# Performance work log

Hardware: AMD Instinct MI355X
Metric: run time of the kernel (lower is better)

The kernel has to match this reference:

```python
import jax, jax.numpy as jnp
import numpy as np

N_SIZE = 8
HIDDEN = 64
CELL = 1.0


def _social_pool(h, coords, mask):
    # h: [N, hid], coords: [N, 2], mask: [N] int
    N = coords.shape[0]
    rel = coords[None, :, :] - coords[:, None, :]            # rel[i, j] = coords[j] - coords[i]
    g = jnp.trunc(rel / CELL).astype(jnp.int32)              # python int() truncates toward zero
    half = N_SIZE // 2
    inb = (jnp.abs(g[..., 0]) <= half - 1) & (jnp.abs(g[..., 1]) <= half - 1)
    eye = jnp.eye(N, dtype=bool)
    m = mask != 0
    valid = inb & (~eye) & m[:, None] & m[None, :]           # [N, N]
    cell_idx = (g[..., 0] + half) * N_SIZE + (g[..., 1] + half)
    seg = jnp.arange(N, dtype=jnp.int32)[:, None] * (N_SIZE * N_SIZE) + jnp.where(valid, cell_idx, 0)
    contrib = jnp.where(valid[..., None], h[None, :, :], jnp.zeros((), h.dtype))  # [N, N, hid]
    H = jax.ops.segment_sum(contrib.reshape(N * N, -1), seg.reshape(-1),
                            num_segments=N * N_SIZE * N_SIZE)
    return H.reshape(N, N_SIZE * N_SIZE * h.shape[-1])


def _forward(X, part_masks, all_h_t, all_c_t, Y, T_pred,
             W_emb, b_emb, W_soc, b_soc, W_ih, b_ih, W_hh, b_hh, W_out, b_out):
    T, N = X.shape[0], X.shape[1]
    masks = part_masks[:, 0, :]                              # [T, N]
    masks_tm3 = jnp.concatenate([jnp.ones((3, N), masks.dtype), masks[:-3]], axis=0)
    ts = jnp.arange(T, dtype=jnp.int32)

    def step(carry, xs):
        h, c = carry
        x_t, mask_t, mask_tm3, y_t, t = xs
        coords = x_t[:, 2:]                                  # [N, 2]
        r = jax.nn.relu(coords @ W_emb + b_emb)              # Phi (dropout inactive in eval)
        H = _social_pool(h, coords, mask_t)
        e = jax.nn.relu(H @ W_soc + b_soc)
        z = jnp.concatenate([r, e], axis=1)
        gates = z @ W_ih + b_ih + h @ W_hh + b_hh            # torch LSTMCell gate order i,f,g,o
        i_g, f_g, g_g, o_g = jnp.split(gates, 4, axis=1)
        c_new = jax.nn.sigmoid(f_g) * c + jax.nn.sigmoid(i_g) * jnp.tanh(g_g)
        h_new = jax.nn.sigmoid(o_g) * jnp.tanh(c_new)
        out = (h_new @ W_out + b_out) * mask_t.astype(h.dtype)[:, None]
        appear = (t > 3) & (mask_t != 0) & (mask_tm3 == 0)
        out = jnp.where(appear[:, None], y_t, out)
        active = t <= T_pred                                 # frames beyond T_pred are skipped
        h2 = jnp.where(active, h_new, h)
        c2 = jnp.where(active, c_new, c)
        out = jnp.where(active, out, jnp.zeros_like(out))
        return (h2, c2), out

    (_, _), outputs = jax.lax.scan(step, (all_h_t, all_c_t), (X, masks, masks_tm3, Y, ts))
    return outputs


def setup_inputs() -> dict:
    key = jax.random.key(0)
    ks = jax.random.split(key, 16)
    T, N = 32, 1024
    inp = {
        "X": jax.random.normal(ks[0], (T, N, 4), jnp.float32),
        "part_masks": jax.random.randint(ks[1], (T, 1, N), 0, 2, jnp.int32),
        "all_h_t": jax.random.normal(ks[2], (N, HIDDEN), jnp.float32),
        "all_c_t": jax.random.normal(ks[3], (N, HIDDEN), jnp.float32),
        "Y": jax.random.normal(ks[4], (T, N, 2), jnp.float32),
        "T_obs": 20,
        "T_pred": 24,
        "W_emb": jax.random.normal(ks[5], (2, 64), jnp.float32) * 0.1,
        "b_emb": jax.random.normal(ks[6], (64,), jnp.float32) * 0.1,
        "W_soc": jax.random.normal(ks[7], (N_SIZE * N_SIZE * HIDDEN, 256), jnp.float32) * 0.02,
        "b_soc": jax.random.normal(ks[8], (256,), jnp.float32) * 0.1,
        "W_ih": jax.random.normal(ks[9], (64 + 256, 4 * HIDDEN), jnp.float32) * 0.05,
        "b_ih": jax.random.normal(ks[10], (4 * HIDDEN,), jnp.float32) * 0.1,
        "W_hh": jax.random.normal(ks[11], (HIDDEN, 4 * HIDDEN), jnp.float32) * 0.05,
        "b_hh": jax.random.normal(ks[12], (4 * HIDDEN,), jnp.float32) * 0.1,
        "W_out": jax.random.normal(ks[13], (HIDDEN, 2), jnp.float32) * 0.1,
        "b_out": jax.random.normal(ks[14], (2,), jnp.float32) * 0.1,
    }
    return inp


def reference(X, part_masks, all_h_t, all_c_t, Y, T_obs, T_pred,
              W_emb, b_emb, W_soc, b_soc, W_ih, b_ih, W_hh, b_hh, W_out, b_out):
    return _forward(X, part_masks, all_h_t, all_c_t, Y, T_pred,
                    W_emb, b_emb, W_soc, b_soc, W_ih, b_ih, W_hh, b_hh, W_out, b_out)
```

## Files before the change

### kernel.cpp

```cpp
#include <hip/hip_runtime.h>
#include <hip/hip_bf16.h>


typedef short bf16x8 __attribute__((ext_vector_type(8)));
typedef float f32x4 __attribute__((ext_vector_type(4)));

__device__ __forceinline__ float u2f(unsigned short u) {
    union { unsigned int i; float f; } v; v.i = ((unsigned int)u) << 16; return v.f;
}
__device__ __forceinline__ unsigned short f2b(float f) {
    __hip_bfloat16 hb = __float2bfloat16(f);
    return *(unsigned short*)&hb;
}
__device__ __forceinline__ float ldin(const void* p, int idx, int isf32) {
    return isf32 ? ((const float*)p)[idx] : u2f(((const unsigned short*)p)[idx]);
}
__device__ __forceinline__ int get_tpred(const int* p) {
    int v = p[0];
    if (v >= 0 && v <= 64) return v;
    float f = ((const float*)p)[0];
    if (f >= 0.f && f <= 64.f) return (int)f;
    float g = u2f(((const unsigned short*)p)[0]);
    if (g >= 0.f && g <= 64.f) return (int)g;
    return 31;
}

__global__ __launch_bounds__(256) void k_detect(const void* __restrict__ Wsoc,
                                                int* __restrict__ flag) {
    __shared__ int f;
    int tid = threadIdx.x;
    if (tid == 0) f = 0;
    __syncthreads();
    const unsigned short* p = (const unsigned short*)Wsoc;
    #pragma unroll
    for (int k = 0; k < 4; k++) {
        float v = u2f(p[tid * 4 + k]);
        if (!(v == v) || fabsf(v) > 1e20f) f = 1;
    }
    __syncthreads();
    if (tid == 0) flag[0] = f;
}

__global__ __launch_bounds__(256) void k_transpose(const void* __restrict__ Wsoc,
                                                   unsigned short* __restrict__ Wt2,
                                                   const int* __restrict__ flag) {
    __shared__ __align__(16) unsigned short tile[32 * 264];
    int isf32 = flag[0];
    int b = blockIdx.x, tid = threadIdx.x;
    int k0 = b * 32;
    if (isf32) {
        const float* W = (const float*)Wsoc;
        #pragma unroll
        for (int p = 0; p < 4; p++) {
            int kk = (tid >> 5) + p * 8;
            int n8 = (tid & 31) * 8;
            #pragma unroll
            for (int q = 0; q < 8; q++)
                tile[kk * 264 + n8 + q] = f2b(W[(k0 + kk) * 256 + n8 + q]);
        }
    } else {
        const unsigned short* W = (const unsigned short*)Wsoc;
        #pragma unroll
        for (int p = 0; p < 4; p++) {
            int kk = (tid >> 5) + p * 8;
            int n8 = (tid & 31) * 8;
            *(uint4*)&tile[kk * 264 + n8] = *(const uint4*)(W + (k0 + kk) * 256 + n8);
        }
    }
    __syncthreads();
    int n = tid;
    unsigned int packed[16];
    #pragma unroll
    for (int q = 0; q < 16; q++) {
        unsigned int lo = tile[(2 * q) * 264 + n];
        unsigned int hi = tile[(2 * q + 1) * 264 + n];
        packed[q] = lo | (hi << 16);
    }
    int craw = k0 >> 6, kk0 = k0 & 63;
    uint4* dst = (uint4*)(Wt2 + (long)craw * 16384 + (long)n * 64 + kk0);
    #pragma unroll
    for (int p = 0; p < 4; p++)
        dst[p] = make_uint4(packed[4*p], packed[4*p+1], packed[4*p+2], packed[4*p+3]);
}

__global__ __launch_bounds__(256) void k_init(void* __restrict__ out,
                                              const void* __restrict__ hin,
                                              const void* __restrict__ cin,
                                              float* __restrict__ h_ws,
                                              float* __restrict__ c_ws,
                                              const int* __restrict__ flag) {
    int isf32 = flag[0];
    int b = blockIdx.x, tid = threadIdx.x;
    if (b < 16) {
        uint4 z = make_uint4(0u, 0u, 0u, 0u);
        uint4* p = (uint4*)out;
        int n16 = isf32 ? 16384 : 8192;
        for (int idx = b * 256 + tid; idx < n16; idx += 4096) p[idx] = z;
    } else {
        int sb = b - 16;
        const void* src = (sb < 16) ? hin : cin;
        float* dst = (sb < 16) ? h_ws : c_ws;
        sb &= 15;
        int base = (sb * 256 + tid) * 16;
        #pragma unroll
        for (int p = 0; p < 16; p++) dst[base + p] = ldin(src, base + p, isf32);
    }
}

__global__ __launch_bounds__(256) void k_codes(const void* __restrict__ X,
                                               const int* __restrict__ masks,
                                               const void* __restrict__ Wemb,
                                               const void* __restrict__ bemb,
                                               const int* __restrict__ Tpred,
                                               const int* __restrict__ flag,
                                               float* __restrict__ r_all,
                                               unsigned short* __restrict__ offs,
                                               unsigned short* __restrict__ ents) {
    int bid = blockIdx.x;
    int t = bid >> 10, i = bid & 1023;
    if (t > get_tpred(Tpred)) return;
    int isf32 = flag[0];
    int tid = threadIdx.x;
    __shared__ int cnt[49];
    __shared__ unsigned short off_s[52];
    float cix, ciy;
    if (isf32) {
        const float* Xf = (const float*)X;
        cix = Xf[(t * 1024 + i) * 4 + 2];
        ciy = Xf[(t * 1024 + i) * 4 + 3];
    } else {
        const unsigned short* Xb = (const unsigned short*)X;
        cix = u2f(Xb[(t * 1024 + i) * 4 + 2]);
        ciy = u2f(Xb[(t * 1024 + i) * 4 + 3]);
    }
    if (tid < 64) {
        float v = ldin(Wemb, tid, isf32) * cix + ldin(Wemb, 64 + tid, isf32) * ciy
                + ldin(bemb, tid, isf32);
        r_all[((long)t * 1024 + i) * 64 + tid] = fmaxf(v, 0.f);
    }
    if (masks[t * 1024 + i] == 0) return;
    if (tid < 49) cnt[tid] = 0;
    __syncthreads();
    int cc[4], rk[4];
    #pragma unroll
    for (int p = 0; p < 4; p++) {
        int j = tid + p * 256;
        cc[p] = -1;
        if (j != i && masks[t * 1024 + j] != 0) {
            float dx, dy;
            if (isf32) {
                const float* Xf = (const float*)X;
                dx = Xf[(t * 1024 + j) * 4 + 2] - cix;
                dy = Xf[(t * 1024 + j) * 4 + 3] - ciy;
            } else {
                const unsigned short* Xb = (const unsigned short*)X;
                dx = u2f(Xb[(t * 1024 + j) * 4 + 2]) - cix;
                dy = u2f(Xb[(t * 1024 + j) * 4 + 3]) - ciy;
            }
            int g0 = (int)dx, g1 = (int)dy;
            if (g0 >= -3 && g0 <= 3 && g1 >= -3 && g1 <= 3) {
                int c = (g0 + 3) * 7 + (g1 + 3);
                cc[p] = c;
                rk[p] = atomicAdd(&cnt[c], 1);
            }
        }
    }
    __syncthreads();
    if (tid == 0) {
        int o = 0;
        #pragma unroll 1
        for (int c = 0; c < 49; c++) { off_s[c] = (unsigned short)o; o += cnt[c]; }
        off_s[49] = (unsigned short)o;
    }
    __syncthreads();
    unsigned short* eb = ents + ((long)t * 1024 + i) * 1024;
    #pragma unroll
    for (int p = 0; p < 4; p++)
        if (cc[p] >= 0)
            eb[off_s[cc[p]] + rk[p]] = (unsigned short)(tid + p * 256);
    if (tid < 50) offs[((long)t * 1024 + i) * 64 + tid] = off_s[tid];
}

__global__ __launch_bounds__(256) void k_pool(const int* __restrict__ masks,
                                              const int* __restrict__ Tpred,
                                              const float* __restrict__ h_ws,
                                              const unsigned short* __restrict__ offs,
                                              const unsigned short* __restrict__ ents,
                                              unsigned short* __restrict__ Hbuf,
                                              int t) {
    if (t > get_tpred(Tpred)) return;
    int i = blockIdx.x, tid = threadIdx.x;
    long hb_base = (long)i * 3136;
    if (masks[t * 1024 + i] == 0) {
        unsigned int* hp = (unsigned int*)(Hbuf + hb_base);
        for (int idx = tid; idx < 1568; idx += 256) hp[idx] = 0u;
        return;
    }
    __shared__ __align__(16) unsigned short el[1024];
    __shared__ unsigned short of[52];
    if (tid < 50) of[tid] = offs[((long)t * 1024 + i) * 64 + tid];
    {
        const uint4* src = (const uint4*)(ents + ((long)t * 1024 + i) * 1024);
        uint4* dst = (uint4*)el;
        if (tid < 128) dst[tid] = src[tid];
    }
    __syncthreads();
    int w = tid >> 6, lane = tid & 63;
    for (int c = w; c < 49; c += 4) {
        int k = of[c], n = of[c + 1];
        float acc = 0.f;
        for (; k + 8 <= n; k += 8) {
            int j0 = el[k], j1 = el[k + 1], j2 = el[k + 2], j3 = el[k + 3];
            int j4 = el[k + 4], j5 = el[k + 5], j6 = el[k + 6], j7 = el[k + 7];
            float v0 = h_ws[j0 * 64 + lane];
            float v1 = h_ws[j1 * 64 + lane];
            float v2 = h_ws[j2 * 64 + lane];
            float v3 = h_ws[j3 * 64 + lane];
            float v4 = h_ws[j4 * 64 + lane];
            float v5 = h_ws[j5 * 64 + lane];
            float v6 = h_ws[j6 * 64 + lane];
            float v7 = h_ws[j7 * 64 + lane];
            acc += ((v0 + v1) + (v2 + v3)) + ((v4 + v5) + (v6 + v7));
        }
        for (; k < n; k++) acc += h_ws[el[k] * 64 + lane];
        Hbuf[hb_base + c * 64 + lane] = f2b(acc);
    }
}

__global__ __launch_bounds__(256) void k_gemm(const unsigned short* __restrict__ Hbuf,
                                              const unsigned short* __restrict__ Wt2,
                                              const int* __restrict__ Tpred,
                                              float* __restrict__ part,
                                              int t) {
    if (t > get_tpred(Tpred)) return;
    int bid = blockIdx.x, tid = threadIdx.x;
    int ch = bid & 3, s = (bid >> 2) & 7, rb = bid >> 5;
    int row0 = rb * 64, col0 = ch * 64;
    int m0 = (49 * s) >> 3, m1 = (49 * (s + 1)) >> 3;
    __shared__ __align__(16) short Asm[2][64 * 72];
    __shared__ __align__(16) short Bsm[2][64 * 72];
    int w = tid >> 6, lane = tid & 63;
    int wrow = (w & 1) * 32, wcol = (w >> 1) * 32;
    int mrow = lane & 15, q = lane >> 4;
    int row = tid >> 2, seg = tid & 3;
    const unsigned short* Arow = Hbuf + (long)(row0 + row) * 3136;
    const long boff = (long)(col0 + row) * 64;
    f32x4 acc[2][2];
    f32x4 zz = {0.f, 0.f, 0.f, 0.f};
    #pragma unroll
    for (int a = 0; a < 2; a++)
        #pragma unroll
        for (int b = 0; b < 2; b++) acc[a][b] = zz;
    uint4 ra0, ra1, rb0, rb1;
    {
        int craw = ((m0 / 7) * 8 + (m0 % 7) + 9);
        const unsigned short* Bc = Wt2 + (long)craw * 16384 + boff;
        ra0 = *(const uint4*)(Arow + m0 * 64 + seg * 8);
        ra1 = *(const uint4*)(Arow + m0 * 64 + (seg + 4) * 8);
        rb0 = *(const uint4*)(Bc + seg * 8);
        rb1 = *(const uint4*)(Bc + (seg + 4) * 8);
        *(uint4*)&Asm[0][row * 72 + seg * 8] = ra0;
        *(uint4*)&Asm[0][row * 72 + (seg + 4) * 8] = ra1;
        *(uint4*)&Bsm[0][row * 72 + seg * 8] = rb0;
        *(uint4*)&Bsm[0][row * 72 + (seg + 4) * 8] = rb1;
    }
    __syncthreads();
    for (int m = m0; m < m1; m++) {
        int p = (m - m0) & 1;
        if (m + 1 < m1) {
            int mm = m + 1;
            int craw = ((mm / 7) * 8 + (mm % 7) + 9);
            const unsigned short* Bc = Wt2 + (long)craw * 16384 + boff;
            ra0 = *(const uint4*)(Arow + mm * 64 + seg * 8);
            ra1 = *(const uint4*)(Arow + mm * 64 + (seg + 4) * 8);
            rb0 = *(const uint4*)(Bc + seg * 8);
            rb1 = *(const uint4*)(Bc + (seg + 4) * 8);
            *(uint4*)&Asm[p ^ 1][row * 72 + seg * 8] = ra0;
            *(uint4*)&Asm[p ^ 1][row * 72 + (seg + 4) * 8] = ra1;
            *(uint4*)&Bsm[p ^ 1][row * 72 + seg * 8] = rb0;
            *(uint4*)&Bsm[p ^ 1][row * 72 + (seg + 4) * 8] = rb1;
        }
        #pragma unroll
        for (int kc = 0; kc < 2; kc++) {
            bf16x8 a0 = *(bf16x8*)&Asm[p][(wrow +      mrow) * 72 + kc * 32 + q * 8];
            bf16x8 a1 = *(bf16x8*)&Asm[p][(wrow + 16 + mrow) * 72 + kc * 32 + q * 8];
            #pragma unroll
            for (int ct = 0; ct < 2; ct++) {
                bf16x8 bv = *(bf16x8*)&Bsm[p][(wcol + ct * 16 + mrow) * 72 + kc * 32 + q * 8];
                acc[0][ct] = __builtin_amdgcn_mfma_f32_16x16x32_bf16(a0, bv, acc[0][ct], 0, 0, 0);
                acc[1][ct] = __builtin_amdgcn_mfma_f32_16x16x32_bf16(a1, bv, acc[1][ct], 0, 0, 0);
            }
        }
        __syncthreads();
    }
    float* ps = part + (long)s * 262144;
    #pragma unroll
    for (int rt = 0; rt < 2; rt++)
        #pragma unroll
        for (int ct = 0; ct < 2; ct++)
            #pragma unroll
            for (int r = 0; r < 4; r++) {
                int grow = row0 + wrow + rt * 16 + q * 4 + r;
                int gcol = col0 + wcol + ct * 16 + mrow;
                ps[grow * 256 + gcol] = acc[rt][ct][r];
            }
}

__global__ __launch_bounds__(1024) void k_cell(const int* __restrict__ masks,
                                               const void* __restrict__ Y,
                                               const void* __restrict__ bsoc,
                                               const void* __restrict__ Wih,
                                               const void* __restrict__ bih,
                                               const void* __restrict__ Whh,
                                               const void* __restrict__ bhh,
                                               const void* __restrict__ Wout,
                                               const void* __restrict__ bout,
                                               const int* __restrict__ Tpred,
                                               const int* __restrict__ flag,
                                               float* __restrict__ h_ws,
                                               float* __restrict__ c_ws,
                                               const float* __restrict__ r_all,
                                               const float* __restrict__ part,
                                               void* __restrict__ out,
                                               int t) {
    if (t > get_tpred(Tpred)) return;
    int isf32 = flag[0];
    int tid = threadIdx.x;
    int r0 = blockIdx.x * 4;
    __shared__ __align__(16) float zT[384][4];
    __shared__ float g2[4][4][256];
    for (int idx = tid; idx < 1536; idx += 1024) {
        int r = idx / 384, k = idx - r * 384;
        int grow = r0 + r;
        float v;
        if (k < 64) {
            v = r_all[((long)t * 1024 + grow) * 64 + k];
        } else if (k < 320) {
            int col = k - 64;
            const float* pp = part + grow * 256 + col;
            float s0 = pp[0 * 262144] + pp[1 * 262144];
            float s1 = pp[2 * 262144] + pp[3 * 262144];
            float s2 = pp[4 * 262144] + pp[5 * 262144];
            float s3 = pp[6 * 262144] + pp[7 * 262144];
            v = fmaxf(ldin(bsoc, col, isf32) + ((s0 + s1) + (s2 + s3)), 0.f);
        } else {
            v = h_ws[grow * 64 + (k - 320)];
        }
        zT[k][r] = v;
    }
    __syncthreads();
    int kh = tid >> 8, col = tid & 255;
    int klo = kh * 96, khi = klo + 96;
    float a0 = 0.f, a1 = 0.f, a2 = 0.f, a3 = 0.f;
    if (isf32) {
        const float* W1 = (const float*)Wih;
        const float* W2 = (const float*)Whh;
        int kmid = khi < 320 ? khi : 320;
        #pragma unroll 8
        for (int k = klo; k < kmid; k++) {
            float wv = W1[(long)k * 256 + col];
            f32x4 zv = *(f32x4*)&zT[k][0];
            a0 += zv[0] * wv; a1 += zv[1] * wv; a2 += zv[2] * wv; a3 += zv[3] * wv;
        }
        int k2 = klo > 320 ? klo : 320;
        #pragma unroll 8
        for (int k = k2; k < khi; k++) {
            float wv = W2[(long)(k - 320) * 256 + col];
            f32x4 zv = *(f32x4*)&zT[k][0];
            a0 += zv[0] * wv; a1 += zv[1] * wv; a2 += zv[2] * wv; a3 += zv[3] * wv;
        }
    } else {
        const unsigned short* W1 = (const unsigned short*)Wih;
        const unsigned short* W2 = (const unsigned short*)Whh;
        int kmid = khi < 320 ? khi : 320;
        #pragma unroll 8
        for (int k = klo; k < kmid; k++) {
            float wv = u2f(W1[(long)k * 256 + col]);
            f32x4 zv = *(f32x4*)&zT[k][0];
            a0 += zv[0] * wv; a1 += zv[1] * wv; a2 += zv[2] * wv; a3 += zv[3] * wv;
        }
        int k2 = klo > 320 ? klo : 320;
        #pragma unroll 8
        for (int k = k2; k < khi; k++) {
            float wv = u2f(W2[(long)(k - 320) * 256 + col]);
            f32x4 zv = *(f32x4*)&zT[k][0];
            a0 += zv[0] * wv; a1 += zv[1] * wv; a2 += zv[2] * wv; a3 += zv[3] * wv;
        }
    }
    g2[kh][0][col] = a0; g2[kh][1][col] = a1;
    g2[kh][2][col] = a2; g2[kh][3][col] = a3;
    __syncthreads();
    if (tid < 256) {
        float bb = ldin(bih, tid, isf32) + ldin(bhh, tid, isf32);
        #pragma unroll
        for (int r = 0; r < 4; r++)
            g2[0][r][tid] = ((g2[0][r][tid] + g2[1][r][tid])
                           + (g2[2][r][tid] + g2[3][r][tid])) + bb;
    }
    __syncthreads();
    if (tid < 256) {
        int row = tid >> 6, u = tid & 63;
        int grow = r0 + row;
        float gi = g2[0][row][u];
        float gf = g2[0][row][64 + u];
        float gg = g2[0][row][128 + u];
        float go = g2[0][row][192 + u];
        float c  = c_ws[grow * 64 + u];
        float si = 1.f / (1.f + __expf(-gi));
        float sf = 1.f / (1.f + __expf(-gf));
        float so = 1.f / (1.f + __expf(-go));
        float cn = sf * c + si * tanhf(gg);
        float hn = so * tanhf(cn);
        c_ws[grow * 64 + u] = cn;
        h_ws[grow * 64 + u] = hn;
        float p0 = hn * ldin(Wout, u * 2 + 0, isf32);
        float p1 = hn * ldin(Wout, u * 2 + 1, isf32);
        #pragma unroll
        for (int o = 32; o >= 1; o >>= 1) {
            p0 += __shfl_xor(p0, o);
            p1 += __shfl_xor(p1, o);
        }
        if (u == 0) {
            int m = masks[t * 1024 + grow];
            float o0 = 0.f, o1 = 0.f;
            if (m != 0) {
                bool appear = (t > 3) && (masks[(t - 3) * 1024 + grow] == 0);
                if (appear) {
                    o0 = ldin(Y, (t * 1024 + grow) * 2 + 0, isf32);
                    o1 = ldin(Y, (t * 1024 + grow) * 2 + 1, isf32);
                } else {
                    o0 = p0 + ldin(bout, 0, isf32);
                    o1 = p1 + ldin(bout, 1, isf32);
                }
            }
            if (!(o0 == o0)) o0 = 0.f;
            if (!(o1 == o1)) o1 = 0.f;
            int ofs = (t * 1024 + grow) * 2;
            if (isf32) {
                ((float*)out)[ofs + 0] = o0;
                ((float*)out)[ofs + 1] = o1;
            } else {
                ((unsigned short*)out)[ofs + 0] = f2b(o0);
                ((unsigned short*)out)[ofs + 1] = f2b(o1);
            }
        }
    }
}

extern "C" void kernel_launch(void* const* d_in, const int* in_sizes, int n_in,
                              void* d_out, int out_size, void* d_ws, size_t ws_size,
                              hipStream_t stream) {
    (void)in_sizes; (void)n_in; (void)out_size; (void)ws_size;
    const void* X     = d_in[0];
    const int*  masks = (const int*)d_in[1];
    const void* h0    = d_in[2];
    const void* c0    = d_in[3];
    const void* Y     = d_in[4];
    const int*  Tpred = (const int*)d_in[6];
    const void* Wemb  = d_in[7];
    const void* bemb  = d_in[8];
    const void* Wsoc  = d_in[9];
    const void* bsoc  = d_in[10];
    const void* Wih   = d_in[11];
    const void* bih   = d_in[12];
    const void* Whh   = d_in[13];
    const void* bhh   = d_in[14];
    const void* Wout  = d_in[15];
    const void* bout  = d_in[16];

    char* ws = (char*)d_ws;
    float*          h_ws  = (float*)(ws + 0);
    float*          c_ws  = (float*)(ws + 262144);
    unsigned short* Wt2   = (unsigned short*)(ws + 1835008);
    unsigned short* Hbuf  = (unsigned short*)(ws + 3932160);
    int*            flag  = (int*)(ws + 11141120);
    float*          part  = (float*)(ws + 16777216);
    float*          r_all = (float*)(ws + 33554432);
    unsigned short* offs  = (unsigned short*)(ws + 41943040);
    unsigned short* ents  = (unsigned short*)(ws + 50331648);

    k_detect<<<1, 256, 0, stream>>>(Wsoc, flag);
    k_transpose<<<128, 256, 0, stream>>>(Wsoc, Wt2, flag);
    k_init<<<48, 256, 0, stream>>>(d_out, h0, c0, h_ws, c_ws, flag);
    k_codes<<<32768, 256, 0, stream>>>(X, masks, Wemb, bemb, Tpred, flag,
                                       r_all, offs, ents);
    for (int t = 0; t < 32; t++) {
        k_pool<<<1024, 256, 0, stream>>>(masks, Tpred, h_ws, offs, ents, Hbuf, t);
        k_gemm<<<512, 256, 0, stream>>>(Hbuf, Wt2, Tpred, part, t);
        k_cell<<<256, 1024, 0, stream>>>(masks, Y, bsoc, Wih, bih, Whh, bhh,
                                         Wout, bout, Tpred, flag, h_ws, c_ws,
                                         r_all, part, d_out, t);
    }
}
```

Baseline: 1.077 ms.

## Skip zeroing masked pool rows, mask them in GEMM, interleave cell gathers

Masked agents no longer have their pooled rows zeroed in k_pool. k_gemm instead reads each block's masks into shared memory and substitutes zeros for A-tile loads of masked rows. k_pool now walks two cells per wave at once to give each wave more independent gather loads in flight. k_codes uses per-wave counters for bucket ranking to cut shared-atomic contention, at the cost of a slightly larger serial prefix pass.

Result: slower. 1.106 ms (+2.7%).

```diff
diff --git a/kernel.cpp b/kernel.cpp
--- a/kernel.cpp
+++ b/kernel.cpp
@@ -121,7 +121,9 @@
     if (t > get_tpred(Tpred)) return;
     int isf32 = flag[0];
     int tid = threadIdx.x;
-    __shared__ int cnt[49];
+    int w = tid >> 6;
+    __shared__ int cnt[4][52];
+    __shared__ unsigned short wb[4][52];
     __shared__ unsigned short off_s[52];
     float cix, ciy;
     if (isf32) {
@@ -139,7 +141,7 @@
         r_all[((long)t * 1024 + i) * 64 + tid] = fmaxf(v, 0.f);
     }
     if (masks[t * 1024 + i] == 0) return;
-    if (tid < 49) cnt[tid] = 0;
+    if (tid < 208) ((int*)cnt)[tid] = 0;
     __syncthreads();
     int cc[4], rk[4];
     #pragma unroll
@@ -161,7 +163,7 @@
             if (g0 >= -3 && g0 <= 3 && g1 >= -3 && g1 <= 3) {
                 int c = (g0 + 3) * 7 + (g1 + 3);
                 cc[p] = c;
-                rk[p] = atomicAdd(&cnt[c], 1);
+                rk[p] = atomicAdd(&cnt[w][c], 1);
             }
         }
     }
@@ -169,7 +171,15 @@
     if (tid == 0) {
         int o = 0;
         #pragma unroll 1
-        for (int c = 0; c < 49; c++) { off_s[c] = (unsigned short)o; o += cnt[c]; }
+        for (int c = 0; c < 49; c++) {
+            off_s[c] = (unsigned short)o;
+            int b0 = o;
+            wb[0][c] = (unsigned short)b0; b0 += cnt[0][c];
+            wb[1][c] = (unsigned short)b0; b0 += cnt[1][c];
+            wb[2][c] = (unsigned short)b0; b0 += cnt[2][c];
+            wb[3][c] = (unsigned short)b0; b0 += cnt[3][c];
+            o = b0;
+        }
         off_s[49] = (unsigned short)o;
     }
     __syncthreads();
@@ -177,7 +187,7 @@
     #pragma unroll
     for (int p = 0; p < 4; p++)
         if (cc[p] >= 0)
-            eb[off_s[cc[p]] + rk[p]] = (unsigned short)(tid + p * 256);
+            eb[wb[w][cc[p]] + rk[p]] = (unsigned short)(tid + p * 256);
     if (tid < 50) offs[((long)t * 1024 + i) * 64 + tid] = off_s[tid];
 }
 
@@ -190,12 +200,8 @@
                                               int t) {
     if (t > get_tpred(Tpred)) return;
     int i = blockIdx.x, tid = threadIdx.x;
+    if (masks[t * 1024 + i] == 0) return;
     long hb_base = (long)i * 3136;
-    if (masks[t * 1024 + i] == 0) {
-        unsigned int* hp = (unsigned int*)(Hbuf + hb_base);
-        for (int idx = tid; idx < 1568; idx += 256) hp[idx] = 0u;
-        return;
-    }
     __shared__ __align__(16) unsigned short el[1024];
     __shared__ unsigned short of[52];
     if (tid < 50) of[tid] = offs[((long)t * 1024 + i) * 64 + tid];
@@ -206,29 +212,52 @@
     }
     __syncthreads();
     int w = tid >> 6, lane = tid & 63;
-    for (int c = w; c < 49; c += 4) {
-        int k = of[c], n = of[c + 1];
-        float acc = 0.f;
-        for (; k + 8 <= n; k += 8) {
-            int j0 = el[k], j1 = el[k + 1], j2 = el[k + 2], j3 = el[k + 3];
-            int j4 = el[k + 4], j5 = el[k + 5], j6 = el[k + 6], j7 = el[k + 7];
-            float v0 = h_ws[j0 * 64 + lane];
-            float v1 = h_ws[j1 * 64 + lane];
-            float v2 = h_ws[j2 * 64 + lane];
-            float v3 = h_ws[j3 * 64 + lane];
-            float v4 = h_ws[j4 * 64 + lane];
-            float v5 = h_ws[j5 * 64 + lane];
-            float v6 = h_ws[j6 * 64 + lane];
-            float v7 = h_ws[j7 * 64 + lane];
-            acc += ((v0 + v1) + (v2 + v3)) + ((v4 + v5) + (v6 + v7));
-        }
-        for (; k < n; k++) acc += h_ws[el[k] * 64 + lane];
-        Hbuf[hb_base + c * 64 + lane] = f2b(acc);
+    for (int c0 = w; c0 < 49; c0 += 8) {
+        int c1 = c0 + 4;
+        bool hasB = (c1 < 49);
+        int kA = of[c0], eA = of[c0 + 1];
+        int kB = hasB ? of[c1] : 0, eB = hasB ? of[c1 + 1] : 0;
+        float aA = 0.f, aB = 0.f;
+        while (kA + 8 <= eA && kB + 8 <= eB) {
+            int ja[8], jb[8];
+            #pragma unroll
+            for (int u = 0; u < 8; u++) { ja[u] = el[kA + u]; jb[u] = el[kB + u]; }
+            float sa = 0.f, sb = 0.f;
+            #pragma unroll
+            for (int u = 0; u < 8; u++) {
+                sa += h_ws[ja[u] * 64 + lane];
+                sb += h_ws[jb[u] * 64 + lane];
+            }
+            aA += sa; aB += sb; kA += 8; kB += 8;
+        }
+        for (; kA + 8 <= eA; kA += 8) {
+            int ja[8];
+            #pragma unroll
+            for (int u = 0; u < 8; u++) ja[u] = el[kA + u];
+            float sa = 0.f;
+            #pragma unroll
+            for (int u = 0; u < 8; u++) sa += h_ws[ja[u] * 64 + lane];
+            aA += sa;
+        }
+        for (; kB + 8 <= eB; kB += 8) {
+            int jb[8];
+            #pragma unroll
+            for (int u = 0; u < 8; u++) jb[u] = el[kB + u];
+            float sb = 0.f;
+            #pragma unroll
+            for (int u = 0; u < 8; u++) sb += h_ws[jb[u] * 64 + lane];
+            aB += sb;
+        }
+        for (; kA < eA; kA++) aA += h_ws[el[kA] * 64 + lane];
+        for (; kB < eB; kB++) aB += h_ws[el[kB] * 64 + lane];
+        Hbuf[hb_base + c0 * 64 + lane] = f2b(aA);
+        if (hasB) Hbuf[hb_base + c1 * 64 + lane] = f2b(aB);
     }
 }
 
 __global__ __launch_bounds__(256) void k_gemm(const unsigned short* __restrict__ Hbuf,
                                               const unsigned short* __restrict__ Wt2,
+                                              const int* __restrict__ masks,
                                               const int* __restrict__ Tpred,
                                               float* __restrict__ part,
                                               int t) {
@@ -239,10 +268,12 @@
     int m0 = (49 * s) >> 3, m1 = (49 * (s + 1)) >> 3;
     __shared__ __align__(16) short Asm[2][64 * 72];
     __shared__ __align__(16) short Bsm[2][64 * 72];
+    __shared__ int maskL[64];
     int w = tid >> 6, lane = tid & 63;
     int wrow = (w & 1) * 32, wcol = (w >> 1) * 32;
     int mrow = lane & 15, q = lane >> 4;
     int row = tid >> 2, seg = tid & 3;
+    if (tid < 64) maskL[tid] = masks[t * 1024 + row0 + tid];
     const unsigned short* Arow = Hbuf + (long)(row0 + row) * 3136;
     const long boff = (long)(col0 + row) * 64;
     f32x4 acc[2][2];
@@ -251,12 +282,15 @@
     for (int a = 0; a < 2; a++)
         #pragma unroll
         for (int b = 0; b < 2; b++) acc[a][b] = zz;
+    __syncthreads();
+    int rmask = maskL[row];
+    uint4 zv4 = make_uint4(0u, 0u, 0u, 0u);
     uint4 ra0, ra1, rb0, rb1;
     {
         int craw = ((m0 / 7) * 8 + (m0 % 7) + 9);
         const unsigned short* Bc = Wt2 + (long)craw * 16384 + boff;
-        ra0 = *(const uint4*)(Arow + m0 * 64 + seg * 8);
-        ra1 = *(const uint4*)(Arow + m0 * 64 + (seg + 4) * 8);
+        ra0 = rmask ? *(const uint4*)(Arow + m0 * 64 + seg * 8) : zv4;
+        ra1 = rmask ? *(const uint4*)(Arow + m0 * 64 + (seg + 4) * 8) : zv4;
         rb0 = *(const uint4*)(Bc + seg * 8);
         rb1 = *(const uint4*)(Bc + (seg + 4) * 8);
         *(uint4*)&Asm[0][row * 72 + seg * 8] = ra0;
@@ -271,8 +305,8 @@
             int mm = m + 1;
             int craw = ((mm / 7) * 8 + (mm % 7) + 9);
             const unsigned short* Bc = Wt2 + (long)craw * 16384 + boff;
-            ra0 = *(const uint4*)(Arow + mm * 64 + seg * 8);
-            ra1 = *(const uint4*)(Arow + mm * 64 + (seg + 4) * 8);
+            ra0 = rmask ? *(const uint4*)(Arow + mm * 64 + seg * 8) : zv4;
+            ra1 = rmask ? *(const uint4*)(Arow + mm * 64 + (seg + 4) * 8) : zv4;
             rb0 = *(const uint4*)(Bc + seg * 8);
             rb1 = *(const uint4*)(Bc + (seg + 4) * 8);
             *(uint4*)&Asm[p ^ 1][row * 72 + seg * 8] = ra0;
@@ -486,7 +520,7 @@
                                        r_all, offs, ents);
     for (int t = 0; t < 32; t++) {
         k_pool<<<1024, 256, 0, stream>>>(masks, Tpred, h_ws, offs, ents, Hbuf, t);
-        k_gemm<<<512, 256, 0, stream>>>(Hbuf, Wt2, Tpred, part, t);
+        k_gemm<<<512, 256, 0, stream>>>(Hbuf, Wt2, masks, Tpred, part, t);
         k_cell<<<256, 1024, 0, stream>>>(masks, Y, bsoc, Wih, bih, Whh, bhh,
                                          Wout, bout, Tpred, flag, h_ws, c_ws,
                                          r_all, part, d_out, t);
```
